# Performance work log

Measured on AMD Instinct MI355X. Metric: run time of the kernel, lower is better.

The kernel has to match this reference:

```python
import jax, jax.numpy as jnp
import numpy as np
from jax import lax

B, L = 2, 2048
DIM, HEADS = 1024, 16
HD = DIM // HEADS            # 64
D_STATE, D_CONV = 16, 4
D_INNER = 2 * DIM            # mamba expand=2
DT_RANK = DIM // 16          # 64


def setup_inputs() -> dict:
    key = jax.random.key(0)
    ks = jax.random.split(key, 12)
    w = lambda k, shape, s=0.02: (jax.random.normal(k, shape, jnp.float32) * s)
    # A initialized as in Mamba: A_log = log(1..d_state) per channel
    A_log = jnp.log(jnp.tile(jnp.arange(1, D_STATE + 1, dtype=jnp.float32), (D_INNER, 1)))
    return {
        "x": jax.random.normal(ks[0], (B, L, DIM), jnp.float32),
        # MultiQueryAttention params (Wqkv: dim -> dim + 2*head_dim)
        "wqkv": w(ks[1], (DIM, DIM + 2 * HD)),
        "bqkv": jnp.zeros((DIM + 2 * HD,), jnp.float32),
        "w_attn_out": w(ks[2], (DIM, DIM)),
        "b_attn_out": jnp.zeros((DIM,), jnp.float32),
        # MambaBlock params
        "w_in": w(ks[3], (DIM, 2 * D_INNER)),          # in_proj (no bias)
        "conv_w": w(ks[4], (D_INNER, D_CONV), 0.1),    # depthwise causal conv
        "conv_b": jnp.zeros((D_INNER,), jnp.float32),
        "w_xproj": w(ks[5], (D_INNER, DT_RANK + 2 * D_STATE)),
        "w_dt": w(ks[6], (DT_RANK, D_INNER)),
        "b_dt": w(ks[7], (D_INNER,), 0.01),
        "A_log": A_log,
        "Dp": jnp.ones((D_INNER,), jnp.float32),
        "w_out": w(ks[8], (D_INNER, DIM)),             # out_proj (no bias)
    }


def _mqa(x, wqkv, bqkv, w_attn_out, b_attn_out):
    b, l, d = x.shape
    qkv = x @ wqkv + bqkv
    q = qkv[..., :DIM].reshape(b, l, HEADS, HD)          # blhd
    k = qkv[..., DIM:DIM + HD]                           # bmd (single shared head)
    v = qkv[..., DIM + HD:]                              # bmd
    scores = jnp.einsum("blhd,bmd->bhlm", q, k) / np.sqrt(HD).astype(np.float32)
    causal = jnp.tril(jnp.ones((l, l), bool))
    scores = jnp.where(causal, scores, jnp.finfo(scores.dtype).min)
    attn = jax.nn.softmax(scores, axis=-1)
    out = jnp.einsum("bhlm,bmd->blhd", attn, v).reshape(b, l, DIM)
    return out @ w_attn_out + b_attn_out


def _mamba(x, w_in, conv_w, conv_b, w_xproj, w_dt, b_dt, A_log, Dp, w_out):
    b, l, d = x.shape
    xr = x @ w_in                                        # (b,l,2*d_inner)
    u0, res = xr[..., :D_INNER], xr[..., D_INNER:]
    # causal depthwise conv1d (torch pads d_conv-1 both sides then slices [:l])
    lhs = u0.transpose(0, 2, 1)                          # (b, d_inner, l)
    rhs = conv_w[:, None, :]                             # (d_inner, 1, d_conv)
    xc = lax.conv_general_dilated(
        lhs, rhs, window_strides=(1,), padding=[(D_CONV - 1, 0)],
        dimension_numbers=("NCH", "OIH", "NCH"), feature_group_count=D_INNER)
    u = jax.nn.silu((xc + conv_b[None, :, None]).transpose(0, 2, 1))  # (b,l,d_inner)

    x_dbl = u @ w_xproj
    delta = jax.nn.softplus(x_dbl[..., :DT_RANK] @ w_dt + b_dt)       # (b,l,d_inner)
    Bm = x_dbl[..., DT_RANK:DT_RANK + D_STATE]                        # (b,l,n)
    Cm = x_dbl[..., DT_RANK + D_STATE:]                               # (b,l,n)
    A = -jnp.exp(A_log)                                               # (d_inner, n)

    def step(h, inp):
        d_t, b_t, c_t, u_t = inp                       # (b,d),(b,n),(b,n),(b,d)
        dA = jnp.exp(d_t[..., None] * A)               # (b,d,n)
        h = dA * h + (d_t * u_t)[..., None] * b_t[:, None, :]
        y = jnp.einsum("bdn,bn->bd", h, c_t)
        return h, y

    xs = (delta.transpose(1, 0, 2), Bm.transpose(1, 0, 2),
          Cm.transpose(1, 0, 2), u.transpose(1, 0, 2))
    h0 = jnp.zeros((b, D_INNER, D_STATE), u.dtype)
    _, ys = lax.scan(step, h0, xs)                     # (l,b,d_inner)
    y = ys.transpose(1, 0, 2) + u * Dp
    y = y * jax.nn.silu(res)
    return y @ w_out


def reference(x, wqkv, bqkv, w_attn_out, b_attn_out, w_in, conv_w, conv_b,
              w_xproj, w_dt, b_dt, A_log, Dp, w_out):
    attended = _mqa(x, wqkv, bqkv, w_attn_out, b_attn_out)
    x1 = attended + x                                   # residual 1
    y = _mamba(x1, w_in, conv_w, conv_b, w_xproj, w_dt, b_dt, A_log, Dp, w_out)
    return y + x1                                       # residual 2
```

## Files before the change

kernel.cpp:

```cpp
#include <hip/hip_runtime.h>

#define L_SEQ   2048
#define BATCH   2
#define NDIM    1024
#define NHEADS  16
#define HD      64
#define DSTATE  16
#define DCONV   4
#define DINNER  2048
#define DTRANK  64
#define CHUNK   32
#define NCHUNK  (L_SEQ / CHUNK)
#define SPLIT_KT 8

typedef short  short8  __attribute__((ext_vector_type(8)));
typedef float  floatx4 __attribute__((ext_vector_type(4)));

#define AS1 __attribute__((address_space(1)))
#define AS3 __attribute__((address_space(3)))

__device__ __forceinline__ float bf2f(ushort u) {
    union { uint i; float f; } v; v.i = ((uint)u) << 16; return v.f;
}
#if defined(__has_builtin) && __has_builtin(__builtin_amdgcn_cvt_pk_bf16_f32)
__device__ __forceinline__ ushort f2bf(float f) {
    auto p = __builtin_amdgcn_cvt_pk_bf16_f32(f, f);
    union { decltype(p) v; ushort u[2]; } cv; cv.v = p;
    return cv.u[0];
}
__device__ __forceinline__ uint pk2bf(float lo, float hi) {
    auto p = __builtin_amdgcn_cvt_pk_bf16_f32(lo, hi);
    union { decltype(p) v; uint u; } cv; cv.v = p;
    return cv.u;
}
#else
__device__ __forceinline__ ushort f2bf(float f) {
    uint x = __float_as_uint(f);
    uint r = (x + 0x7fffu + ((x >> 16) & 1u)) >> 16;
    return (ushort)r;
}
__device__ __forceinline__ uint pk2bf(float lo, float hi) {
    return ((uint)f2bf(hi) << 16) | (uint)f2bf(lo);
}
#endif
__device__ __forceinline__ float silu_f(float x) {
    return x / (1.f + __expf(-x));
}
__device__ __forceinline__ void gld_lds16(const void* g, void* l) {
    __builtin_amdgcn_global_load_lds((const AS1 uint*)g, (AS3 uint*)l, 16, 0, 0);
}
__device__ __forceinline__ float cvt_one(const void* s, int i, int f) {
    return f ? ((const float*)s)[i] : bf2f(((const ushort*)s)[i]);
}

__global__ __launch_bounds__(256) void prep_kernel(
    const void* __restrict__ x_raw,
    const void* __restrict__ wqkv, const void* __restrict__ wao,
    const void* __restrict__ win,  const void* __restrict__ wxp,
    const void* __restrict__ wdt,  const void* __restrict__ wout,
    const void* __restrict__ bqkv, const void* __restrict__ bao,
    const void* __restrict__ convw, const void* __restrict__ convb,
    const void* __restrict__ bdt,  const void* __restrict__ Alog,
    const void* __restrict__ Dp,
    ushort* __restrict__ x_b, ushort* __restrict__ wqkv_t,
    ushort* __restrict__ wao_t, ushort* __restrict__ win_t,
    ushort* __restrict__ wxp_t, ushort* __restrict__ wdt_t,
    ushort* __restrict__ wout_t,
    float* __restrict__ bqkv_f, float* __restrict__ bao_f,
    float* __restrict__ convw_f, float* __restrict__ convb_f,
    float* __restrict__ bdt_f, float* __restrict__ Alog_f,
    float* __restrict__ Dp_f, int* __restrict__ flag)
{
    __shared__ int cnt;
    __shared__ float tile[32][33];
    if (threadIdx.x == 0) cnt = 0;
    __syncthreads();
    {
        ushort w = ((const ushort*)x_raw)[threadIdx.x];
        int e = (w >> 7) & 0xff;
        if (w != 0 && (e < 100 || e > 140)) atomicAdd(&cnt, 1);
    }
    __syncthreads();
    const int f = (cnt >= 16) ? 1 : 0;
    if (blockIdx.x == 0 && threadIdx.x == 0) *flag = f;

    int id = blockIdx.x;
    if (id < 16384) {
        int i = id * 256 + threadIdx.x;
        x_b[i] = f2bf(cvt_one(x_raw, i, f));
        return;
    }
    id -= 16384;

    const void* src = nullptr; ushort* dst = nullptr; int K = 0, N = 0;
    if (id < 1152)                     { src = wqkv; dst = wqkv_t; K = 1024; N = 1152; }
    else if ((id -= 1152) < 1024)      { src = wao;  dst = wao_t;  K = 1024; N = 1024; }
    else if ((id -= 1024) < 4096)      { src = win;  dst = win_t;  K = 1024; N = 4096; }
    else if ((id -= 4096) < 192)       { src = wxp;  dst = wxp_t;  K = 2048; N = 96;   }
    else if ((id -= 192)  < 128)       { src = wdt;  dst = wdt_t;  K = 64;   N = 2048; }
    else if ((id -= 128)  < 2048)      { src = wout; dst = wout_t; K = 2048; N = 1024; }
    else {
        id -= 2048;
        if (id < 256) {
            wxp_t[(size_t)96 * DINNER + id * 256 + threadIdx.x] = 0;
        } else {
            int i = (id - 256) * 256 + threadIdx.x;
            if      (i < 1152)   bqkv_f[i]          = cvt_one(bqkv,  i,          f);
            else if (i < 2176)   bao_f[i - 1152]    = cvt_one(bao,   i - 1152,   f);
            else if (i < 10368)  convw_f[i - 2176]  = cvt_one(convw, i - 2176,   f);
            else if (i < 12416)  convb_f[i - 10368] = cvt_one(convb, i - 10368,  f);
            else if (i < 14464)  bdt_f[i - 12416]   = cvt_one(bdt,   i - 12416,  f);
            else if (i < 47232)  Alog_f[i - 14464]  = -__expf(cvt_one(Alog, i - 14464, f));
            else if (i < 49280)  Dp_f[i - 47232]    = cvt_one(Dp,    i - 47232,  f);
        }
        return;
    }

    const int ntn = N / 32;
    const int n0 = (id % ntn) * 32, k0 = (id / ntn) * 32;
    const int tx = threadIdx.x & 31, ty = threadIdx.x >> 5;
    #pragma unroll
    for (int r = 0; r < 4; ++r) {
        size_t o = (size_t)(k0 + ty + r * 8) * N + n0 + tx;
        tile[ty + r * 8][tx] = cvt_one(src, (int)o, f);
    }
    __syncthreads();
    #pragma unroll
    for (int r = 0; r < 4; ++r) {
        int n = n0 + ty + r * 8;
        dst[(size_t)n * K + k0 + tx] = f2bf(tile[tx][ty + r * 8]);
    }
}

__global__ __launch_bounds__(256) void gemm128(
    const ushort* __restrict__ A, int lda,
    const ushort* __restrict__ Wt,
    const float* __restrict__ bias,
    const ushort* __restrict__ resb,
    ushort* __restrict__ outb, float* __restrict__ outf,
    const int* __restrict__ dtflag,
    int N, int K, int act, int klen, float* __restrict__ psum, int swap)
{
    __shared__ __align__(16) char smem[34048];
    ushort* As = (ushort*)smem;
    ushort* Bs = (ushort*)(smem + 16384);

    const int tid  = threadIdx.x;
    const int wave = tid >> 6;
    const int lane = tid & 63;
    const int wm = (wave >> 1) * 64;
    const int wn = (wave & 1) * 64;
    const int fm = lane & 15;
    const int quad = lane >> 4;

    int bx = blockIdx.x, by = blockIdx.y;
    {
        const int gx = gridDim.x;
        const int nwg = gx * gridDim.y;
        const int id = by * gx + bx;
        const int qq = nwg >> 3;
        const int sid = (id & 7) * qq + (id >> 3);
        bx = sid % gx; by = sid / gx;
    }
    const int m0 = (swap ? bx : by) * 128;
    const int n0 = (swap ? by : bx) * 128;

    floatx4 acc[4][4];
    #pragma unroll
    for (int i = 0; i < 4; ++i)
        #pragma unroll
        for (int j = 0; j < 4; ++j) acc[i][j] = (floatx4){0.f, 0.f, 0.f, 0.f};

    int rowv[4], kgv[4];
    #pragma unroll
    for (int j = 0; j < 4; ++j) {
        int c = wave * 256 + j * 64 + lane;
        rowv[j] = c >> 3;
        kgv[j]  = (((c & 7) ^ ((c >> 3) & 7))) * 8;
    }

    const int kbeg = psum ? (blockIdx.z * klen) : 0;
    const int kend = kbeg + klen;

    for (int k0 = kbeg; k0 < kend; k0 += 64) {
        #pragma unroll
        for (int j = 0; j < 4; ++j)
            gld_lds16(A  + (size_t)(m0 + rowv[j]) * lda + k0 + kgv[j],
                      &As[(wave * 256 + j * 64) * 8]);
        #pragma unroll
        for (int j = 0; j < 4; ++j)
            gld_lds16(Wt + (size_t)(n0 + rowv[j]) * K   + k0 + kgv[j],
                      &Bs[(wave * 256 + j * 64) * 8]);
        __syncthreads();

        #pragma unroll
        for (int h = 0; h < 2; ++h) {
            short8 af[4], bf[4];
            #pragma unroll
            for (int i = 0; i < 4; ++i) {
                int row = wm + i * 16 + fm;
                int slot = (h * 4 + quad) ^ (row & 7);
                af[i] = *(const short8*)&As[row * 64 + slot * 8];
            }
            #pragma unroll
            for (int j = 0; j < 4; ++j) {
                int row = wn + j * 16 + fm;
                int slot = (h * 4 + quad) ^ (row & 7);
                bf[j] = *(const short8*)&Bs[row * 64 + slot * 8];
            }
            #pragma unroll
            for (int i = 0; i < 4; ++i)
                #pragma unroll
                for (int j = 0; j < 4; ++j)
                    acc[i][j] = __builtin_amdgcn_mfma_f32_16x16x32_bf16(af[i], bf[j], acc[i][j], 0, 0, 0);
        }
        __syncthreads();
    }

    if (psum) {
        int mgrid = swap ? gridDim.x : gridDim.y;
        float* po = psum + (size_t)blockIdx.z * ((size_t)mgrid * 128) * N;
        #pragma unroll
        for (int j = 0; j < 4; ++j) {
            int col = n0 + wn + j * 16 + fm;
            #pragma unroll
            for (int i = 0; i < 4; ++i) {
                int rowb = m0 + wm + i * 16 + quad * 4;
                #pragma unroll
                for (int r = 0; r < 4; ++r)
                    po[(size_t)(rowb + r) * N + col] = acc[i][j][r];
            }
        }
        return;
    }

    const int flagv = dtflag ? *dtflag : 0;
    const bool wf = dtflag ? (flagv != 0) : (outf != nullptr);
    float* Cs = (float*)smem;
    const int lrw = (wm >> 1) + quad * 4;
    #pragma unroll
    for (int p = 0; p < 2; ++p) {
        #pragma unroll
        for (int ih = 0; ih < 2; ++ih) {
            const int i = 2 * p + ih;
            #pragma unroll
            for (int j = 0; j < 4; ++j) {
                float bvv = bias ? bias[n0 + wn + j * 16 + fm] : 0.f;
                #pragma unroll
                for (int r = 0; r < 4; ++r) {
                    float v = acc[i][j][r] + bvv;
                    if (act == 1)
                        v = fmaxf(v, 0.f) + __logf(1.f + __expf(-fabsf(v)));
                    Cs[(lrw + ih * 16 + r) * 132 + wn + j * 16 + fm] = v;
                }
            }
        }
        __syncthreads();
        #pragma unroll
        for (int g = 0; g < 4; ++g) {
            const int lr   = g * 16 + (tid >> 4);
            const int colc = (tid & 15) * 8;
            const int grow = m0 + (lr >> 5) * 64 + (2 * p + ((lr >> 4) & 1)) * 16 + (lr & 15);
            const size_t o = (size_t)grow * N + n0 + colc;
            floatx4 v0 = *(const floatx4*)&Cs[lr * 132 + colc];
            floatx4 v1 = *(const floatx4*)&Cs[lr * 132 + colc + 4];
            float vv[8] = {v0[0], v0[1], v0[2], v0[3], v1[0], v1[1], v1[2], v1[3]};
            if (resb) {
                short8 rs = *(const short8*)&resb[o];
                #pragma unroll
                for (int k = 0; k < 8; ++k) vv[k] += bf2f((ushort)rs[k]);
            }
            if (wf) {
                *(floatx4*)&outf[o]     = (floatx4){vv[0], vv[1], vv[2], vv[3]};
                *(floatx4*)&outf[o + 4] = (floatx4){vv[4], vv[5], vv[6], vv[7]};
            } else {
                short8 ov;
                #pragma unroll
                for (int k = 0; k < 8; ++k) ov[k] = (short)f2bf(vv[k]);
                *(short8*)&outb[o] = ov;
            }
        }
        __syncthreads();
    }
}

__global__ __launch_bounds__(256) void combine_xdbl(
    const float* __restrict__ psum, ushort* __restrict__ xdbl)
{
    int idx = blockIdx.x * 256 + threadIdx.x;
    int row = idx / 96, col = idx - row * 96;
    float s = 0.f;
    #pragma unroll
    for (int z = 0; z < 8; ++z)
        s += psum[(size_t)z * 4096 * 128 + row * 128 + col];
    xdbl[idx] = f2bf(s);
}

__global__ __launch_bounds__(256) void flash_attn_split(
    const ushort* __restrict__ qkv, ushort* __restrict__ att,
    ushort* __restrict__ partO, float* __restrict__ partL)
{
    __shared__ __align__(16) ushort Ks[64 * 72];
    __shared__ __align__(16) ushort Vt[64 * 72];

    const int id  = blockIdx.x;
    const int e   = id >> 3;
    const int hgb = id & 7;
    const int hg  = hgb >> 1;
    const int b   = hgb & 1;
    int tile, s;
    if (e < 104) {
        if      (e < 50)  { s = 0; tile = 63 - e; }
        else if (e < 84)  { s = 1; tile = 63 - (e - 50); }
        else if (e < 102) { s = 2; tile = 63 - (e - 84); }
        else              { s = 3; tile = 63 - (e - 102); }
    } else {
        const int rem = e - 104;
        const int w   = 7 - (rem >> 3);
        s    = (rem & 7) >> 1;
        tile = 2 * (8 * s + w) - 2 + (rem & 1);
    }

    const int q0 = tile * 32;
    const int nkv = (q0 >> 6) + 1;
    const int nsplit = (nkv + SPLIT_KT - 1) / SPLIT_KT;
    const int kt0 = s * SPLIT_KT;
    const int kt1 = (nkv < kt0 + SPLIT_KT) ? nkv : (kt0 + SPLIT_KT);

    const int tid  = threadIdx.x;
    const int wave = tid >> 6;
    const int lane = tid & 63;
    const int fm   = lane & 15;
    const int quad = lane >> 4;
    const int h    = hg * 4 + wave;

    const int srow = tid >> 3;
    const int scol = (tid & 7) * 8;
    const int vsw  = (tid & 7) << 3;

    const int addrA = (fm + (quad & 1) * 32) * 4;
    const int addrB = addrA + 64;
    const bool jlo_sel = (quad < 2);

    short8 qf[2][2];
    #pragma unroll
    for (int i = 0; i < 2; ++i)
        #pragma unroll
        for (int kh = 0; kh < 2; ++kh)
            qf[i][kh] = *(const short8*)(qkv +
                (size_t)(b * L_SEQ + q0 + i * 16 + fm) * 1152 + h * HD + kh * 32 + quad * 8);

    floatx4 acc[2][4];
    float l_lane[2];
    #pragma unroll
    for (int i = 0; i < 2; ++i) {
        #pragma unroll
        for (int j = 0; j < 4; ++j) acc[i][j] = (floatx4){0.f, 0.f, 0.f, 0.f};
        l_lane[i] = 0.f;
    }

    short8 kreg[2], vreg[2];
    {
        const int kv0 = kt0 * 64;
        #pragma unroll
        for (int pass = 0; pass < 2; ++pass) {
            int row = srow + pass * 32;
            const ushort* kp = qkv + (size_t)(b * L_SEQ + kv0 + row) * 1152 + NDIM + scol;
            kreg[pass] = *(const short8*)kp;
            vreg[pass] = *(const short8*)(kp + HD);
        }
    }

    for (int kt = kt0; kt < kt1; ++kt) {
        const int kv0 = kt * 64;
        __syncthreads();
        #pragma unroll
        for (int pass = 0; pass < 2; ++pass) {
            int row = srow + pass * 32;
            *(short8*)&Ks[row * 72 + scol] = kreg[pass];
            int mw = row ^ vsw;
            #pragma unroll
            for (int i2 = 0; i2 < 8; ++i2) Vt[(scol + i2) * 72 + mw] = (ushort)vreg[pass][i2];
        }
        __syncthreads();

        if (kt + 1 < kt1) {
            const int kv0n = (kt + 1) * 64;
            #pragma unroll
            for (int pass = 0; pass < 2; ++pass) {
                int row = srow + pass * 32;
                const ushort* kp = qkv + (size_t)(b * L_SEQ + kv0n + row) * 1152 + NDIM + scol;
                kreg[pass] = *(const short8*)kp;
                vreg[pass] = *(const short8*)(kp + HD);
            }
        }

        floatx4 spT[4][2];
        __builtin_amdgcn_s_setprio(1);
        #pragma unroll
        for (int j = 0; j < 4; ++j) {
            short8 kf0 = *(const short8*)&Ks[(j * 16 + fm) * 72 + quad * 8];
            short8 kf1 = *(const short8*)&Ks[(j * 16 + fm) * 72 + 32 + quad * 8];
            #pragma unroll
            for (int i = 0; i < 2; ++i) {
                floatx4 z = (floatx4){0.f, 0.f, 0.f, 0.f};
                z = __builtin_amdgcn_mfma_f32_16x16x32_bf16(kf0, qf[i][0], z, 0, 0, 0);
                z = __builtin_amdgcn_mfma_f32_16x16x32_bf16(kf1, qf[i][1], z, 0, 0, 0);
                spT[j][i] = z;
            }
        }
        __builtin_amdgcn_s_setprio(0);

        const bool diag = (kt == nkv - 1);
        #pragma unroll
        for (int j = 0; j < 4; ++j)
            #pragma unroll
            for (int i = 0; i < 2; ++i) {
                #pragma unroll
                for (int r = 0; r < 4; ++r) {
                    float p = __expf(spT[j][i][r] * 0.125f);
                    if (diag) {
                        int kvg = kv0 + j * 16 + quad * 4 + r;
                        int qg  = q0 + i * 16 + fm;
                        if (kvg > qg) p = 0.f;
                    }
                    spT[j][i][r] = p;
                    l_lane[i] += p;
                }
            }

        uint w0[4][2], w1[4][2];
        #pragma unroll
        for (int j = 0; j < 4; ++j)
            #pragma unroll
            for (int i = 0; i < 2; ++i) {
                w0[j][i] = pk2bf(spT[j][i][0], spT[j][i][1]);
                w1[j][i] = pk2bf(spT[j][i][2], spT[j][i][3]);
            }

        short8 pf[2][2];
        #pragma unroll
        for (int i = 0; i < 2; ++i)
            #pragma unroll
            for (int kh = 0; kh < 2; ++kh) {
                const int jl = kh * 2, jh = kh * 2 + 1;
                uint a0 = (uint)__builtin_amdgcn_ds_bpermute(addrA, (int)w0[jl][i]);
                uint a1 = (uint)__builtin_amdgcn_ds_bpermute(addrA, (int)w0[jh][i]);
                uint b0 = (uint)__builtin_amdgcn_ds_bpermute(addrA, (int)w1[jl][i]);
                uint b1 = (uint)__builtin_amdgcn_ds_bpermute(addrA, (int)w1[jh][i]);
                uint c0 = (uint)__builtin_amdgcn_ds_bpermute(addrB, (int)w0[jl][i]);
                uint c1 = (uint)__builtin_amdgcn_ds_bpermute(addrB, (int)w0[jh][i]);
                uint d0 = (uint)__builtin_amdgcn_ds_bpermute(addrB, (int)w1[jl][i]);
                uint d1 = (uint)__builtin_amdgcn_ds_bpermute(addrB, (int)w1[jh][i]);
                union { uint u[4]; short8 s; } cv;
                cv.u[0] = jlo_sel ? a0 : a1;
                cv.u[1] = jlo_sel ? b0 : b1;
                cv.u[2] = jlo_sel ? c0 : c1;
                cv.u[3] = jlo_sel ? d0 : d1;
                pf[i][kh] = cv.s;
            }

        __builtin_amdgcn_s_setprio(1);
        #pragma unroll
        for (int dj = 0; dj < 4; ++dj) {
            int d = dj * 16 + fm;
            int sw8 = ((d >> 3) & 7) << 3;
            short8 vf0 = *(const short8*)&Vt[d * 72 + ((quad * 8) ^ sw8)];
            short8 vf1 = *(const short8*)&Vt[d * 72 + ((32 + quad * 8) ^ sw8)];
            #pragma unroll
            for (int i = 0; i < 2; ++i) {
                acc[i][dj] = __builtin_amdgcn_mfma_f32_16x16x32_bf16(pf[i][0], vf0, acc[i][dj], 0, 0, 0);
                acc[i][dj] = __builtin_amdgcn_mfma_f32_16x16x32_bf16(pf[i][1], vf1, acc[i][dj], 0, 0, 0);
            }
        }
        __builtin_amdgcn_s_setprio(0);
    }

    #pragma unroll
    for (int i = 0; i < 2; ++i) {
        float rs = l_lane[i];
        rs += __shfl_xor(rs, 16);
        rs += __shfl_xor(rs, 32);
        l_lane[i] = rs;
    }

    if (nsplit == 1) {
        #pragma unroll
        for (int i = 0; i < 2; ++i) {
            float inv[4];
            #pragma unroll
            for (int r = 0; r < 4; ++r)
                inv[r] = 1.f / __shfl(l_lane[i], quad * 4 + r, 16);
            #pragma unroll
            for (int dj = 0; dj < 4; ++dj)
                #pragma unroll
                for (int r = 0; r < 4; ++r) {
                    int q = q0 + i * 16 + quad * 4 + r;
                    att[(size_t)(b * L_SEQ + q) * NDIM + h * HD + dj * 16 + fm] =
                        f2bf(acc[i][dj][r] * inv[r]);
                }
        }
    } else {
        size_t pbase = ((size_t)((s * 2 + b) * 16 + h)) * L_SEQ;
        #pragma unroll
        for (int i = 0; i < 2; ++i)
            #pragma unroll
            for (int dj = 0; dj < 4; ++dj)
                #pragma unroll
                for (int r = 0; r < 4; ++r) {
                    int q = q0 + i * 16 + quad * 4 + r;
                    partO[(pbase + q) * 64 + dj * 16 + fm] = f2bf(acc[i][dj][r]);
                }
        if (lane < 16) {
            #pragma unroll
            for (int i = 0; i < 2; ++i)
                partL[pbase + q0 + i * 16 + fm] = l_lane[i];
        }
    }
}

__global__ __launch_bounds__(256) void attn_combine(
    const ushort* __restrict__ partO, const float* __restrict__ partL,
    ushort* __restrict__ att)
{
    int gid = blockIdx.x * 256 + threadIdx.x;
    int t8 = gid & 7;
    int row = gid >> 3;
    int q  = 512 + (row % 1536);
    int bh = row / 1536;
    int b = bh >> 4, h = bh & 15;
    int nsplit = (((q >> 5) >> 1) + 1 + SPLIT_KT - 1) / SPLIT_KT;

    float sum[8] = {0.f, 0.f, 0.f, 0.f, 0.f, 0.f, 0.f, 0.f};
    float L = 0.f;
    for (int s = 0; s < nsplit; ++s) {
        size_t pbase = ((size_t)((s * 2 + b) * 16 + h)) * L_SEQ + q;
        L += partL[pbase];
        short8 o = *(const short8*)&partO[pbase * 64 + t8 * 8];
        #pragma unroll
        for (int k = 0; k < 8; ++k) sum[k] += bf2f((ushort)o[k]);
    }
    float inv = 1.f / L;
    short8 outv;
    #pragma unroll
    for (int k = 0; k < 8; ++k) outv[k] = (short)f2bf(sum[k] * inv);
    *(short8*)&att[((size_t)(b * L_SEQ + q)) * NDIM + h * HD + t8 * 8] = outv;
}

__global__ __launch_bounds__(256) void conv_silu(
    const ushort* __restrict__ xr, const float* __restrict__ conv_w,
    const float* __restrict__ conv_b, ushort* __restrict__ u)
{
    const int c   = ((blockIdx.x & 7) << 8) + threadIdx.x;
    const int bl0 = (blockIdx.x >> 3) << 4;
    const int l0  = bl0 & (L_SEQ - 1);

    const floatx4 wv = *(const floatx4*)&conv_w[c * DCONV];
    const float bias = conv_b[c];

    float xv[19];
    #pragma unroll
    for (int t = 0; t < 19; ++t) {
        int ls = l0 - 3 + t;
        xv[t] = (ls >= 0)
              ? bf2f(xr[(size_t)(bl0 - 3 + t) * (2 * DINNER) + c])
              : 0.f;
    }

    #pragma unroll
    for (int t = 0; t < 16; ++t) {
        float a = bias + xv[t] * wv[0] + xv[t + 1] * wv[1]
                       + xv[t + 2] * wv[2] + xv[t + 3] * wv[3];
        u[(size_t)(bl0 + t) * DINNER + c] = f2bf(silu_f(a));
    }
}

__global__ __launch_bounds__(256) void scan_phase1(
    const ushort* __restrict__ delta, const ushort* __restrict__ u,
    const ushort* __restrict__ xdbl, const float* __restrict__ negA,
    float* __restrict__ Hend, float* __restrict__ Sdt)
{
    const int idx = blockIdx.x * 256 + threadIdx.x;
    const int d = idx & (DINNER - 1);
    const int b = (idx >> 11) & (BATCH - 1);
    const int c = idx >> 12;

    float Av[DSTATE], h[DSTATE];
    #pragma unroll
    for (int n = 0; n < DSTATE; ++n) {
        Av[n] = negA[d * DSTATE + n];
        h[n] = 0.f;
    }

    const int t0 = c * CHUNK;
    size_t bd = ((size_t)b * L_SEQ + t0) * DINNER + d;
    size_t bx = ((size_t)b * L_SEQ + t0) * 96 + DTRANK;
    float sdt = 0.f;

    for (int t = 0; t < CHUNK; ++t) {
        float dt = bf2f(delta[bd]);
        float uv = bf2f(u[bd]);
        sdt += dt;
        float du = dt * uv;
        short8 B0 = *(const short8*)&xdbl[bx];
        short8 B1 = *(const short8*)&xdbl[bx + 8];
        #pragma unroll
        for (int n = 0; n < 8; ++n)
            h[n] = __expf(dt * Av[n]) * h[n] + du * bf2f((ushort)B0[n]);
        #pragma unroll
        for (int n = 0; n < 8; ++n)
            h[8 + n] = __expf(dt * Av[8 + n]) * h[8 + n] + du * bf2f((ushort)B1[n]);
        bd += DINNER; bx += 96;
    }

    size_t ho = (((size_t)c * BATCH + b) * DINNER + d) * DSTATE;
    #pragma unroll
    for (int n = 0; n < DSTATE; n += 4)
        *(floatx4*)&Hend[ho + n] = (floatx4){h[n], h[n + 1], h[n + 2], h[n + 3]};
    Sdt[((size_t)c * BATCH + b) * DINNER + d] = sdt;
}

__global__ __launch_bounds__(256) void scan_phase2(
    float* __restrict__ H, const float* __restrict__ Sdt,
    const float* __restrict__ negA)
{
    const int idx = blockIdx.x * 256 + threadIdx.x;
    const int n = idx & (DSTATE - 1);
    const int d = (idx >> 4) & (DINNER - 1);
    const int b = idx >> 15;

    const float Av = negA[d * DSTATE + n];
    float hin = 0.f;
    for (int c = 0; c < NCHUNK; ++c) {
        size_t o  = (((size_t)c * BATCH + b) * DINNER + d) * DSTATE + n;
        float e   = H[o];
        float dAc = __expf(Av * Sdt[((size_t)c * BATCH + b) * DINNER + d]);
        H[o] = hin;
        hin = dAc * hin + e;
    }
}

__global__ __launch_bounds__(256) void scan_phase3(
    const ushort* __restrict__ delta, const ushort* __restrict__ u,
    const ushort* __restrict__ xdbl, const float* __restrict__ negA,
    const float* __restrict__ Hin, const float* __restrict__ Dp,
    const ushort* __restrict__ xr, ushort* __restrict__ yb)
{
    const int idx = blockIdx.x * 256 + threadIdx.x;
    const int d = idx & (DINNER - 1);
    const int b = (idx >> 11) & (BATCH - 1);
    const int c = idx >> 12;

    float Av[DSTATE], h[DSTATE];
    size_t ho = (((size_t)c * BATCH + b) * DINNER + d) * DSTATE;
    #pragma unroll
    for (int n = 0; n < DSTATE; n += 4) {
        floatx4 hv = *(const floatx4*)&Hin[ho + n];
        h[n] = hv[0]; h[n + 1] = hv[1]; h[n + 2] = hv[2]; h[n + 3] = hv[3];
    }
    #pragma unroll
    for (int n = 0; n < DSTATE; ++n)
        Av[n] = negA[d * DSTATE + n];

    const float Dpd = Dp[d];
    const int t0 = c * CHUNK;
    size_t bd = ((size_t)b * L_SEQ + t0) * DINNER + d;
    size_t bx = ((size_t)b * L_SEQ + t0) * 96 + DTRANK;
    size_t br = ((size_t)b * L_SEQ + t0) * (2 * DINNER) + DINNER + d;

    for (int t = 0; t < CHUNK; ++t) {
        float dt = bf2f(delta[bd]);
        float uv = bf2f(u[bd]);
        float du = dt * uv;
        short8 B0 = *(const short8*)&xdbl[bx];
        short8 B1 = *(const short8*)&xdbl[bx + 8];
        short8 C0 = *(const short8*)&xdbl[bx + 16];
        short8 C1 = *(const short8*)&xdbl[bx + 24];
        float y = 0.f;
        #pragma unroll
        for (int n = 0; n < 8; ++n) {
            h[n] = __expf(dt * Av[n]) * h[n] + du * bf2f((ushort)B0[n]);
            y += h[n] * bf2f((ushort)C0[n]);
        }
        #pragma unroll
        for (int n = 0; n < 8; ++n) {
            h[8 + n] = __expf(dt * Av[8 + n]) * h[8 + n] + du * bf2f((ushort)B1[n]);
            y += h[8 + n] * bf2f((ushort)C1[n]);
        }
        float yv = y + uv * Dpd;
        float r  = bf2f(xr[br]);
        yb[bd] = f2bf(yv * silu_f(r));
        bd += DINNER; bx += 96; br += 2 * DINNER;
    }
}

extern "C" void kernel_launch(void* const* d_in, const int* in_sizes, int n_in,
                              void* d_out, int out_size, void* d_ws, size_t ws_size,
                              hipStream_t stream) {
    const void* x_raw      = d_in[0];
    const void* wqkv_raw   = d_in[1];
    const void* bqkv_raw   = d_in[2];
    const void* wao_raw    = d_in[3];
    const void* bao_raw    = d_in[4];
    const void* win_raw    = d_in[5];
    const void* convw_raw  = d_in[6];
    const void* convb_raw  = d_in[7];
    const void* wxp_raw    = d_in[8];
    const void* wdt_raw    = d_in[9];
    const void* bdt_raw    = d_in[10];
    const void* Alog_raw   = d_in[11];
    const void* Dp_raw     = d_in[12];
    const void* wout_raw   = d_in[13];

    const int M = BATCH * L_SEQ;

    char* p = (char*)d_ws;
    size_t off = 0;
    auto A_ = [&](size_t bytes) { void* q = p + off; off += (bytes + 255) & ~255ull; return q; };

    ushort* x_b    = (ushort*)A_((size_t)M * NDIM * 2);
    ushort* wqkv_t = (ushort*)A_((size_t)NDIM * 1152 * 2);
    ushort* wao_t  = (ushort*)A_((size_t)NDIM * NDIM * 2);
    ushort* win_t  = (ushort*)A_((size_t)NDIM * 4096 * 2);
    float*  psum   = (float*)x_b;
    ushort* yb     = x_b;
    float*  Sdt    = (float*)(x_b + (size_t)M * DINNER);

    ushort* qkv    = (ushort*)A_((size_t)M * 1152 * 2);
    ushort* att    = (ushort*)A_((size_t)M * NDIM * 2);
    float*  Hend   = (float*)qkv;

    ushort* delta_b = (ushort*)A_((size_t)M * DINNER * 2);

    ushort* wxp_t  = (ushort*)A_((size_t)128 * DINNER * 2);
    ushort* wdt_t  = (ushort*)A_((size_t)DTRANK * DINNER * 2);
    ushort* wout_t = (ushort*)A_((size_t)DINNER * NDIM * 2);
    float*  bqkv_f = (float*)A_(1152 * 4);
    float*  bao_f  = (float*)A_(NDIM * 4);
    float*  convw_f= (float*)A_((size_t)DINNER * DCONV * 4);
    float*  convb_f= (float*)A_(DINNER * 4);
    float*  bdt_f  = (float*)A_(DINNER * 4);
    float*  Alog_f = (float*)A_((size_t)DINNER * DSTATE * 4);
    float*  Dp_f   = (float*)A_(DINNER * 4);
    int*    flag   = (int*)A_(256);
    ushort* x1b    = (ushort*)A_((size_t)M * NDIM * 2);
    ushort* xr     = (ushort*)A_((size_t)M * 4096 * 2);
    ushort* u      = (ushort*)A_((size_t)M * DINNER * 2);
    ushort* xdbl   = (ushort*)A_((size_t)M * 96 * 2);

    ushort* partO = xr;
    float*  partL = (float*)u;

    dim3 blk(256);

    prep_kernel<<<dim3(25473), blk, 0, stream>>>(
        x_raw, wqkv_raw, wao_raw, win_raw, wxp_raw, wdt_raw, wout_raw,
        bqkv_raw, bao_raw, convw_raw, convb_raw, bdt_raw, Alog_raw, Dp_raw,
        x_b, wqkv_t, wao_t, win_t, wxp_t, wdt_t, wout_t,
        bqkv_f, bao_f, convw_f, convb_f, bdt_f, Alog_f, Dp_f, flag);

    gemm128<<<dim3(1152 / 128, M / 128), blk, 0, stream>>>(
        x_b, NDIM, wqkv_t, bqkv_f, nullptr, qkv, nullptr, nullptr, 1152, NDIM, 0, NDIM, nullptr, 0);

    flash_attn_split<<<dim3(1280), blk, 0, stream>>>(
        qkv, att, partO, partL);
    attn_combine<<<dim3(1536), blk, 0, stream>>>(partO, partL, att);

    gemm128<<<dim3(NDIM / 128, M / 128), blk, 0, stream>>>(
        att, NDIM, wao_t, bao_f, x_b, x1b, nullptr, nullptr, NDIM, NDIM, 0, NDIM, nullptr, 0);

    gemm128<<<dim3(M / 128, 4096 / 128), blk, 0, stream>>>(
        x1b, NDIM, win_t, nullptr, nullptr, xr, nullptr, nullptr, 4096, NDIM, 0, NDIM, nullptr, 1);

    conv_silu<<<dim3((M / 16) * (DINNER / 256)), blk, 0, stream>>>(xr, convw_f, convb_f, u);

    gemm128<<<dim3(1, M / 128, 8), blk, 0, stream>>>(
        u, DINNER, wxp_t, nullptr, nullptr, nullptr, nullptr, nullptr, 128, DINNER, 0, DINNER / 8, psum, 0);
    combine_xdbl<<<dim3(M * 96 / 256), blk, 0, stream>>>(psum, xdbl);

    gemm128<<<dim3(DINNER / 128, M / 128), blk, 0, stream>>>(
        xdbl, 96, wdt_t, bdt_f, nullptr, delta_b, nullptr, nullptr, DINNER, DTRANK, 1, DTRANK, nullptr, 0);

    scan_phase1<<<dim3(NCHUNK * BATCH * DINNER / 256), blk, 0, stream>>>(
        delta_b, u, xdbl, Alog_f, Hend, Sdt);
    scan_phase2<<<dim3(BATCH * DINNER * DSTATE / 256), blk, 0, stream>>>(
        Hend, Sdt, Alog_f);
    scan_phase3<<<dim3(NCHUNK * BATCH * DINNER / 256), blk, 0, stream>>>(
        delta_b, u, xdbl, Alog_f, Hend, Dp_f, xr, yb);

    gemm128<<<dim3(M / 128, NDIM / 128), blk, 0, stream>>>(
        yb, DINNER, wout_t, nullptr, x1b, (ushort*)d_out, (float*)d_out, flag, NDIM, DINNER, 0, DINNER, nullptr, 1);
}
```

Measured before the change: 453.3 us.

## Double-buffer GEMM LDS tiles and batch chunk loads in scan phase2

```diff
diff --git a/kernel.cpp b/kernel.cpp
--- a/kernel.cpp
+++ b/kernel.cpp
@@ -141,9 +141,7 @@
     const int* __restrict__ dtflag,
     int N, int K, int act, int klen, float* __restrict__ psum, int swap)
 {
-    __shared__ __align__(16) char smem[34048];
-    ushort* As = (ushort*)smem;
-    ushort* Bs = (ushort*)(smem + 16384);
+    __shared__ __align__(16) char smem[65536];
 
     const int tid  = threadIdx.x;
     const int wave = tid >> 6;
@@ -182,7 +180,9 @@
     const int kbeg = psum ? (blockIdx.z * klen) : 0;
     const int kend = kbeg + klen;
 
-    for (int k0 = kbeg; k0 < kend; k0 += 64) {
+    auto stage = [&](int buf, int k0) {
+        ushort* As = (ushort*)(smem + buf * 32768);
+        ushort* Bs = (ushort*)(smem + buf * 32768 + 16384);
         #pragma unroll
         for (int j = 0; j < 4; ++j)
             gld_lds16(A  + (size_t)(m0 + rowv[j]) * lda + k0 + kgv[j],
@@ -191,7 +191,16 @@
         for (int j = 0; j < 4; ++j)
             gld_lds16(Wt + (size_t)(n0 + rowv[j]) * K   + k0 + kgv[j],
                       &Bs[(wave * 256 + j * 64) * 8]);
-        __syncthreads();
+    };
+
+    stage(0, kbeg);
+    __syncthreads();
+
+    int cur = 0;
+    for (int k0 = kbeg; k0 < kend; k0 += 64) {
+        if (k0 + 64 < kend) stage(cur ^ 1, k0 + 64);
+        const ushort* As = (const ushort*)(smem + cur * 32768);
+        const ushort* Bs = (const ushort*)(smem + cur * 32768 + 16384);
 
         #pragma unroll
         for (int h = 0; h < 2; ++h) {
@@ -215,6 +224,7 @@
                     acc[i][j] = __builtin_amdgcn_mfma_f32_16x16x32_bf16(af[i], bf[j], acc[i][j], 0, 0, 0);
         }
         __syncthreads();
+        cur ^= 1;
     }
 
     if (psum) {
@@ -630,13 +640,26 @@
     const int b = idx >> 15;
 
     const float Av = negA[d * DSTATE + n];
+    const size_t hstride = (size_t)BATCH * DINNER * DSTATE;
+    const size_t sstride = (size_t)BATCH * DINNER;
+    const size_t ho0 = ((size_t)b * DINNER + d) * DSTATE + n;
+    const size_t so0 = (size_t)b * DINNER + d;
+
     float hin = 0.f;
-    for (int c = 0; c < NCHUNK; ++c) {
-        size_t o  = (((size_t)c * BATCH + b) * DINNER + d) * DSTATE + n;
-        float e   = H[o];
-        float dAc = __expf(Av * Sdt[((size_t)c * BATCH + b) * DINNER + d]);
-        H[o] = hin;
-        hin = dAc * hin + e;
+    for (int c0 = 0; c0 < NCHUNK; c0 += 8) {
+        float e[8], dAc[8];
+        #pragma unroll
+        for (int k = 0; k < 8; ++k) {
+            e[k]   = H[ho0 + (size_t)(c0 + k) * hstride];
+            dAc[k] = Sdt[so0 + (size_t)(c0 + k) * sstride];
+        }
+        #pragma unroll
+        for (int k = 0; k < 8; ++k) dAc[k] = __expf(Av * dAc[k]);
+        #pragma unroll
+        for (int k = 0; k < 8; ++k) {
+            H[ho0 + (size_t)(c0 + k) * hstride] = hin;
+            hin = dAc[k] * hin + e[k];
+        }
     }
 }
 
```

Result: faster. 427.4 us (-5.7%).
